# Kernel tuning notes

Hardware: AMD Instinct MI355X
Metric: run time of the kernel (lower is better)

The kernel has to match this reference:

```python
import jax, jax.numpy as jnp
import numpy as np
import math

D_MODEL = 1024
NUM_HEADS = 16
MAX_LEN = 2048
B, S = 2, 2048


def setup_inputs() -> dict:
    key = jax.random.key(0)
    ks = jax.random.split(key, 6)
    w_scale = 1.0 / math.sqrt(D_MODEL)  # ~xavier
    return {
        "x": jax.random.normal(ks[0], (B, S, D_MODEL), dtype=jnp.float32),
        "Wq": jax.random.normal(ks[1], (D_MODEL, D_MODEL), dtype=jnp.float32) * w_scale,
        "bq": jnp.zeros((D_MODEL,), dtype=jnp.float32),
        "Wk": jax.random.normal(ks[2], (D_MODEL, D_MODEL), dtype=jnp.float32) * w_scale,
        "bk": jnp.zeros((D_MODEL,), dtype=jnp.float32),
        "Wv": jax.random.normal(ks[3], (D_MODEL, D_MODEL), dtype=jnp.float32) * w_scale,
        "bv": jnp.zeros((D_MODEL,), dtype=jnp.float32),
        "Wo": jax.random.normal(ks[4], (D_MODEL, D_MODEL), dtype=jnp.float32) * w_scale,
        "bo": jnp.zeros((D_MODEL,), dtype=jnp.float32),
        "Er": jax.random.normal(ks[5], (MAX_LEN, D_MODEL // NUM_HEADS), dtype=jnp.float32),
    }


def reference(x, Wq, bq, Wk, bk, Wv, bv, Wo, bo, Er):
    Bsz, Sl, Dm = x.shape
    H = NUM_HEADS
    dqk = Dm // H

    def split_heads(z):
        # [B,S,D] -> [B,H,S,dqk]
        return z.reshape(Bsz, Sl, H, dqk).transpose(0, 2, 1, 3)

    Q = split_heads(x @ Wq.T + bq)
    K = split_heads(x @ Wk.T + bk)
    V = split_heads(x @ Wv.T + bv)

    Er_sl = Er[MAX_LEN - Sl:, :]  # [S, dqk]
    # Faithful to source: contract over d -> [B,H,S], unsqueeze last dim
    QEr = jnp.einsum('bhld,ld->bhl', Q, Er_sl)[..., None]  # [B,H,S,1]
    # skew(): pad left by 1 on last dim, reshape, drop first row
    padded = jnp.pad(QEr, ((0, 0), (0, 0), (0, 0), (1, 0)))  # [B,H,S,2]
    Srel = padded.reshape(Bsz, H, 2, Sl)[:, :, 1:, :]  # [B,H,1,S]

    QK_t = jnp.einsum('bhld,bhmd->bhlm', Q, K)  # [B,H,S,S]
    attn_scores = (QK_t + Srel) / math.sqrt(dqk)

    causal = jnp.tril(jnp.ones((Sl, Sl), dtype=bool))  # [S,S]
    attn_scores = jnp.where(causal[None, None], attn_scores, -jnp.inf)

    attn_probs = jax.nn.softmax(attn_scores, axis=-1)
    attn_out = jnp.einsum('bhlm,bhmd->bhld', attn_probs, V)  # [B,H,S,dqk]
    attn_out = attn_out.transpose(0, 2, 1, 3).reshape(Bsz, Sl, Dm)
    return attn_out @ Wo.T + bo  # dropout omitted (eval mode)
```

## Files before the change

kernel.cpp:

```cpp
#include <hip/hip_runtime.h>
#include <hip/hip_bf16.h>

#define D_MODEL 1024
#define NHEAD 16
#define DH 64
#define BSZ 2
#define SEQ 2048
#define MROWS (BSZ*SEQ)
#define SCL_Q 0.1803368801111204f
#define CHSZ 17408

typedef __attribute__((ext_vector_type(4))) float f32x4;
typedef __attribute__((ext_vector_type(8))) __bf16 bf16x8;
typedef __attribute__((ext_vector_type(8))) unsigned short u16x8;

__device__ __forceinline__ float b2f(unsigned short u) {
    union { unsigned int i; float f; } v; v.i = ((unsigned int)u) << 16; return v.f;
}
__device__ __forceinline__ unsigned short f2b(float f) {
    union { float f; unsigned int i; } v; v.f = f;
    unsigned int u = v.i;
    u += 0x7fffu + ((u >> 16) & 1u);
    return (unsigned short)(u >> 16);
}

#define GLDS16(gptr, lptr) \
    __builtin_amdgcn_global_load_lds((__attribute__((address_space(1))) void*)(gptr), \
                                     (__attribute__((address_space(3))) void*)(lptr), 16, 0, 0)

__global__ __launch_bounds__(256) void cvt5(
    const float* __restrict__ sx,
    const float* __restrict__ s1, const float* __restrict__ s2,
    const float* __restrict__ s3, const float* __restrict__ s4,
    unsigned short* __restrict__ dx,
    unsigned short* __restrict__ d1, unsigned short* __restrict__ d2,
    unsigned short* __restrict__ d3, unsigned short* __restrict__ d4)
{
    const int seg = blockIdx.y;
    const float* src; unsigned short* dst; int n4;
    if (seg == 0)      { src = sx; dst = dx; n4 = MROWS*D_MODEL/4; }
    else if (seg == 1) { src = s1; dst = d1; n4 = D_MODEL*D_MODEL/4; }
    else if (seg == 2) { src = s2; dst = d2; n4 = D_MODEL*D_MODEL/4; }
    else if (seg == 3) { src = s3; dst = d3; n4 = D_MODEL*D_MODEL/4; }
    else               { src = s4; dst = d4; n4 = D_MODEL*D_MODEL/4; }
    int i = blockIdx.x * 256 + threadIdx.x;
    int stride = gridDim.x * 256;
    for (; i < n4; i += stride) {
        float4 v = ((const float4*)src)[i];
        ushort4 o;
        o.x = f2b(v.x); o.y = f2b(v.y); o.z = f2b(v.z); o.w = f2b(v.w);
        ((ushort4*)dst)[i] = o;
    }
}

__global__ __launch_bounds__(256) void gemm_qkv(
    const unsigned short* __restrict__ X,
    const unsigned short* __restrict__ Wq, const unsigned short* __restrict__ Wk,
    const unsigned short* __restrict__ Wv,
    const float* __restrict__ bq, const float* __restrict__ bk, const float* __restrict__ bv,
    unsigned short* __restrict__ Qo, unsigned short* __restrict__ Ko, unsigned short* __restrict__ Vo)
{
    __shared__ unsigned short lsA[2][128*32];
    __shared__ unsigned short lsB[2][128*32];
    const int tid = threadIdx.x;
    const int z = blockIdx.z;
    const unsigned short* W = (z==0) ? Wq : (z==1) ? Wk : Wv;
    const float* bias = (z==0) ? bq : (z==1) ? bk : bv;
    unsigned short* Out = (z==0) ? Qo : (z==1) ? Ko : Vo;
    const int tM = blockIdx.y * 128;
    const int tN = blockIdx.x * 128;
    const int w = tid >> 6, lane = tid & 63;
    const int wr = w >> 1, wc = w & 1;
    const int lr = lane & 15, lk = lane >> 4;
    const f32x4 fz = {0.f, 0.f, 0.f, 0.f};
    f32x4 acc[4][4];
    #pragma unroll
    for (int m = 0; m < 4; m++)
        #pragma unroll
        for (int n = 0; n < 4; n++) acc[m][n] = fz;

    const int e0 = tid, e1 = 256 + tid;
    const int r0 = e0 >> 2, c0 = ((e0 & 3) ^ (r0 & 3)) * 8;
    const int r1 = e1 >> 2, c1 = ((e1 & 3) ^ (r1 & 3)) * 8;

#define GEMM_STAGE(buf, k0_) do { \
        GLDS16(X + (size_t)(tM + r0) * D_MODEL + (k0_) + c0, &lsA[buf][e0 * 8]); \
        GLDS16(X + (size_t)(tM + r1) * D_MODEL + (k0_) + c1, &lsA[buf][e1 * 8]); \
        GLDS16(W + (size_t)(tN + r0) * D_MODEL + (k0_) + c0, &lsB[buf][e0 * 8]); \
        GLDS16(W + (size_t)(tN + r1) * D_MODEL + (k0_) + c1, &lsB[buf][e1 * 8]); \
    } while (0)

    GEMM_STAGE(0, 0);
    __syncthreads();
    int cur = 0;
    for (int k0 = 0; k0 < D_MODEL; k0 += 32) {
        if (k0 + 32 < D_MODEL) GEMM_STAGE(cur ^ 1, k0 + 32);
        bf16x8 af[4], bfr[4];
        #pragma unroll
        for (int m = 0; m < 4; m++) {
            int row = wr*64 + m*16 + lr;
            af[m] = *(const bf16x8*)&lsA[cur][row*32 + ((lk ^ (row & 3)) * 8)];
        }
        #pragma unroll
        for (int n = 0; n < 4; n++) {
            int row = wc*64 + n*16 + lr;
            bfr[n] = *(const bf16x8*)&lsB[cur][row*32 + ((lk ^ (row & 3)) * 8)];
        }
        #pragma unroll
        for (int m = 0; m < 4; m++)
            #pragma unroll
            for (int n = 0; n < 4; n++)
                acc[m][n] = __builtin_amdgcn_mfma_f32_16x16x32_bf16(af[m], bfr[n], acc[m][n], 0, 0, 0);
        __syncthreads();
        cur ^= 1;
    }
#undef GEMM_STAGE
    const float qscl = (z == 0) ? SCL_Q : 1.0f;
    #pragma unroll
    for (int m = 0; m < 4; m++) {
        int ibase = tM + wr*64 + m*16 + lk*4;
        #pragma unroll
        for (int n = 0; n < 4; n++) {
            int j = tN + wc*64 + n*16 + lr;
            float bj = bias[j];
            int h = j >> 6, d = j & 63;
            #pragma unroll
            for (int r = 0; r < 4; r++) {
                int row = ibase + r;
                int b = row >> 11, s = row & 2047;
                Out[((size_t)(b*NHEAD + h) * SEQ + s) * DH + d] = f2b((acc[m][n][r] + bj) * qscl);
            }
        }
    }
}

__global__ __launch_bounds__(512) void gemm_out(
    const unsigned short* __restrict__ X, const unsigned short* __restrict__ W,
    const float* __restrict__ bias, float* __restrict__ Out)
{
    __shared__ unsigned short lsA[2][128*32];
    __shared__ unsigned short lsB[2][64*32];
    const int tid = threadIdx.x;
    const int tM = blockIdx.y * 128;
    const int tN = blockIdx.x * 64;
    const int w = tid >> 6, lane = tid & 63;
    const int wr = w >> 1, wc = w & 1;
    const int lr = lane & 15, lk = lane >> 4;
    const f32x4 fz = {0.f, 0.f, 0.f, 0.f};
    f32x4 acc[2][2];
    #pragma unroll
    for (int m = 0; m < 2; m++)
        #pragma unroll
        for (int n = 0; n < 2; n++) acc[m][n] = fz;

    const int ra = tid >> 2, ca = ((tid & 3) ^ (ra & 3)) * 8;
    const int eb = tid & 255;
    const int rb = eb >> 2, cb = ((eb & 3) ^ (rb & 3)) * 8;

#define OUT_STAGE(buf, k0_) do { \
        GLDS16(X + (size_t)(tM + ra) * D_MODEL + (k0_) + ca, &lsA[buf][tid * 8]); \
        if (tid < 256) GLDS16(W + (size_t)(tN + rb) * D_MODEL + (k0_) + cb, &lsB[buf][eb * 8]); \
    } while (0)

    OUT_STAGE(0, 0);
    __syncthreads();
    int cur = 0;
    for (int k0 = 0; k0 < D_MODEL; k0 += 32) {
        if (k0 + 32 < D_MODEL) OUT_STAGE(cur ^ 1, k0 + 32);
        bf16x8 af[2], bfr[2];
        #pragma unroll
        for (int m = 0; m < 2; m++) {
            int row = wr*32 + m*16 + lr;
            af[m] = *(const bf16x8*)&lsA[cur][row*32 + ((lk ^ (row & 3)) * 8)];
        }
        #pragma unroll
        for (int n = 0; n < 2; n++) {
            int row = wc*32 + n*16 + lr;
            bfr[n] = *(const bf16x8*)&lsB[cur][row*32 + ((lk ^ (row & 3)) * 8)];
        }
        #pragma unroll
        for (int m = 0; m < 2; m++)
            #pragma unroll
            for (int n = 0; n < 2; n++)
                acc[m][n] = __builtin_amdgcn_mfma_f32_16x16x32_bf16(af[m], bfr[n], acc[m][n], 0, 0, 0);
        __syncthreads();
        cur ^= 1;
    }
#undef OUT_STAGE
    #pragma unroll
    for (int m = 0; m < 2; m++) {
        int ibase = tM + wr*32 + m*16 + lk*4;
        #pragma unroll
        for (int n = 0; n < 2; n++) {
            int j = tN + wc*32 + n*16 + lr;
            float bj = bias[j];
            #pragma unroll
            for (int r = 0; r < 4; r++)
                Out[(size_t)(ibase + r) * D_MODEL + j] = acc[m][n][r] + bj;
        }
    }
}

__global__ __launch_bounds__(256) void vtrans(const unsigned short* __restrict__ V,
                                              unsigned short* __restrict__ Vt) {
    __shared__ unsigned short t[64][80];
    const int bh = blockIdx.y;
    const int s0 = blockIdx.x * 64;
    const int tid = threadIdx.x;
    #pragma unroll
    for (int i = 0; i < 2; i++) {
        int e = i*256 + tid;
        int r = e >> 3, c = e & 7;
        u16x8 v = *(const u16x8*)&V[((size_t)bh * SEQ + s0 + r) * DH + c*8];
        *(u16x8*)&t[r][c*8] = v;
    }
    __syncthreads();
    #pragma unroll
    for (int i = 0; i < 2; i++) {
        int e = i*256 + tid;
        int d = e >> 3, c = e & 7;
        u16x8 o;
        #pragma unroll
        for (int j = 0; j < 8; j++) o[j] = t[c*8 + j][d];
        *(u16x8*)&Vt[((size_t)bh * DH + d) * SEQ + s0 + c*8] = o;
    }
}

__global__ __launch_bounds__(256) void qer_k(const unsigned short* __restrict__ Q,
                                             const float* __restrict__ Er,
                                             float* __restrict__ qer) {
    int gw = blockIdx.x * 4 + (threadIdx.x >> 6);
    int lane = threadIdx.x & 63;
    int l = gw & (SEQ - 1);
    float p = b2f(Q[(size_t)gw * DH + lane]) * Er[l * DH + lane];
    #pragma unroll
    for (int m = 32; m >= 1; m >>= 1) p += __shfl_xor(p, m, 64);
    if (lane == 0) qer[gw] = p;
}

__global__ __launch_bounds__(512) void attn_k(
    const unsigned short* __restrict__ Q, const unsigned short* __restrict__ Kg,
    const unsigned short* __restrict__ Vt, const float* __restrict__ qer,
    unsigned short* __restrict__ Om, char* __restrict__ part)
{
    __shared__ unsigned short lsK[2][64*64];
    __shared__ unsigned short lsV[2][64*64];
    __shared__ unsigned short lsP[128*64];
    const unsigned char tab[24] = {
        (7<<2),        (15<<2)|2, (15<<2)|3, (14<<2)|2, (14<<2)|3,
        (6<<2),        (13<<2)|2, (13<<2)|3, (12<<2)|2, (12<<2)|3,
        (5<<2),        (11<<2)|2, (11<<2)|3, (10<<2)|2, (10<<2)|3,
        (4<<2),        (9<<2)|2,  (9<<2)|3,  (8<<2)|2,  (8<<2)|3,
        (3<<2), (2<<2), (1<<2), (0<<2)
    };
    const int id = blockIdx.x;
    const int bh = id & 31;
    const int v = tab[id >> 5];
    const int j = v >> 2;
    const bool split = (v >> 1) & 1;
    const int half = v & 1;
    const int kt0 = (split && half) ? (j + 1) : 0;
    const int ktN = (split && !half) ? (j + 1) : (2*j + 2);
    const int b = bh >> 4, h = bh & 15;
    const int tid = threadIdx.x;
    const int w = tid >> 6, lane = tid & 63;
    const int lr = lane & 15, lk = lane >> 4;
    const int q = w*16 + lr;
    const int qrow = j*128 + q;
    const f32x4 fz = {0.f, 0.f, 0.f, 0.f};

    const unsigned short* Qrow = Q + ((size_t)bh * SEQ + qrow) * DH;
    bf16x8 bq0 = *(const bf16x8*)&Qrow[lk*8];
    bf16x8 bq1 = *(const bf16x8*)&Qrow[32 + lk*8];

    const int sr = tid >> 3, sc = ((tid & 7) ^ (sr & 7)) * 8;
    const unsigned short* kst = Kg + ((size_t)bh * SEQ + kt0*64 + sr) * DH + sc;
    const unsigned short* vst = Vt + ((size_t)bh * DH + sr) * SEQ + kt0*64 + sc;
    const float* qb = qer + (size_t)bh * SEQ + 1024 + kt0*32 + lk*2;

#define ATTN_STAGE(buf) do { \
        GLDS16(kst, &lsK[buf][tid * 8]); kst += 64*DH; \
        GLDS16(vst, &lsV[buf][tid * 8]); vst += 64; \
    } while (0)

    f32x4 o[4];
    #pragma unroll
    for (int df = 0; df < 4; df++) o[df] = fz;
    float mrun = -3.0e38f, lsum = 0.0f;

    ATTN_STAGE(0);
    __syncthreads();
    int cur = 0;

    for (int kt = kt0; kt < ktN; kt++) {
        if (kt + 1 < ktN) ATTN_STAGE(cur ^ 1);
        float2 bv[4];
        #pragma unroll
        for (int kf = 0; kf < 4; kf++) bv[kf] = *(const float2*)(qb + kf*8);
        qb += 32;
        float st[4][4];
        __builtin_amdgcn_s_setprio(1);
        #pragma unroll
        for (int kf = 0; kf < 4; kf++) {
            int row = kf*16 + lr;
            bf16x8 a0 = *(const bf16x8*)&lsK[cur][row*64 + ((lk ^ (row & 7)) * 8)];
            bf16x8 a1 = *(const bf16x8*)&lsK[cur][row*64 + (((4 + lk) ^ (row & 7)) * 8)];
            f32x4 zv = fz;
            zv = __builtin_amdgcn_mfma_f32_16x16x32_bf16(a0, bq0, zv, 0, 0, 0);
            zv = __builtin_amdgcn_mfma_f32_16x16x32_bf16(a1, bq1, zv, 0, 0, 0);
            st[kf][0] = zv[0];
            st[kf][1] = zv[1] + bv[kf].x;
            st[kf][2] = zv[2];
            st[kf][3] = zv[3] + bv[kf].y;
        }
        __builtin_amdgcn_s_setprio(0);
        if (kt >= 2*j) {
            #pragma unroll
            for (int kf = 0; kf < 4; kf++) {
                int kg0 = kt*64 + kf*16 + lk*4;
                #pragma unroll
                for (int r = 0; r < 4; r++)
                    if (kg0 + r > qrow) st[kf][r] = -3.0e38f;
            }
        }
        float pm = st[0][0];
        #pragma unroll
        for (int kf = 0; kf < 4; kf++)
            #pragma unroll
            for (int r = 0; r < 4; r++) pm = fmaxf(pm, st[kf][r]);
        pm = fmaxf(pm, __shfl_xor(pm, 16, 64));
        pm = fmaxf(pm, __shfl_xor(pm, 32, 64));
        if (pm > mrun + 8.0f) {
            float sc8 = exp2f(mrun - pm);
            mrun = pm;
            lsum *= sc8;
            #pragma unroll
            for (int df = 0; df < 4; df++)
                #pragma unroll
                for (int r = 0; r < 4; r++) o[df][r] *= sc8;
        }
        float p[4][4];
        float rs = 0.0f;
        #pragma unroll
        for (int kf = 0; kf < 4; kf++)
            #pragma unroll
            for (int r = 0; r < 4; r++) {
                p[kf][r] = exp2f(st[kf][r] - mrun);
                rs += p[kf][r];
            }
        rs += __shfl_xor(rs, 16, 64);
        rs += __shfl_xor(rs, 32, 64);
        lsum += rs;
        #pragma unroll
        for (int kf = 0; kf < 4; kf++) {
            union { __hip_bfloat162 h2[2]; unsigned long long u; } pk;
            pk.h2[0] = __float22bfloat162_rn(float2{p[kf][0], p[kf][1]});
            pk.h2[1] = __float22bfloat162_rn(float2{p[kf][2], p[kf][3]});
            *(unsigned long long*)&lsP[q*64 + ((((kf<<2)|lk) ^ ((lr&7)<<1))<<2)] = pk.u;
        }
        bf16x8 pb0 = *(const bf16x8*)&lsP[q*64 + ((lk ^ (lr&7))<<3)];
        bf16x8 pb1 = *(const bf16x8*)&lsP[q*64 + (((4+lk) ^ (lr&7))<<3)];
        __builtin_amdgcn_s_setprio(1);
        #pragma unroll
        for (int df = 0; df < 4; df++) {
            int row = df*16 + lr;
            bf16x8 v0 = *(const bf16x8*)&lsV[cur][row*64 + ((lk ^ (row & 7)) * 8)];
            bf16x8 v1 = *(const bf16x8*)&lsV[cur][row*64 + (((4 + lk) ^ (row & 7)) * 8)];
            o[df] = __builtin_amdgcn_mfma_f32_16x16x32_bf16(v0, pb0, o[df], 0, 0, 0);
            o[df] = __builtin_amdgcn_mfma_f32_16x16x32_bf16(v1, pb1, o[df], 0, 0, 0);
        }
        __builtin_amdgcn_s_setprio(0);
        __syncthreads();
        cur ^= 1;
    }
#undef ATTN_STAGE
    if (split) {
        char* cb = part + (size_t)((bh*8 + (j - 8))*2 + half) * CHSZ;
        unsigned short* ob = (unsigned short*)cb;
        #pragma unroll
        for (int df = 0; df < 4; df++) {
            ushort4 ov;
            ov.x = f2b(o[df][0]); ov.y = f2b(o[df][1]);
            ov.z = f2b(o[df][2]); ov.w = f2b(o[df][3]);
            *(ushort4*)&ob[q*64 + df*16 + lk*4] = ov;
        }
        float* ml = (float*)(cb + 16384);
        if (lk == 0) { ml[q] = mrun; ml[128 + q] = lsum; }
    } else {
        float inv = 1.0f / lsum;
        #pragma unroll
        for (int df = 0; df < 4; df++) {
            ushort4 ov;
            ov.x = f2b(o[df][0] * inv);
            ov.y = f2b(o[df][1] * inv);
            ov.z = f2b(o[df][2] * inv);
            ov.w = f2b(o[df][3] * inv);
            *(ushort4*)&Om[((size_t)(b * SEQ + qrow)) * D_MODEL + h*64 + df*16 + lk*4] = ov;
        }
    }
}

__global__ __launch_bounds__(256) void attn_merge(const char* __restrict__ part,
                                                  unsigned short* __restrict__ Om)
{
    const int bh = blockIdx.x & 31, jj = blockIdx.x >> 5;
    const int b = bh >> 4, h = bh & 15, j = 8 + jj;
    const char* c0 = part + (size_t)((bh*8 + jj)*2) * CHSZ;
    const char* c1 = c0 + CHSZ;
    const unsigned short* o0 = (const unsigned short*)c0;
    const unsigned short* o1 = (const unsigned short*)c1;
    const float* ml0 = (const float*)(c0 + 16384);
    const float* ml1 = (const float*)(c1 + 16384);
    const int t = threadIdx.x;
    const int q = t >> 1, dh = (t & 1) * 32;
    float m0 = ml0[q], l0 = ml0[128 + q];
    float m1 = ml1[q], l1 = ml1[128 + q];
    float M = fmaxf(m0, m1);
    float w0 = exp2f(m0 - M), w1 = exp2f(m1 - M);
    float inv = 1.0f / (l0 * w0 + l1 * w1);
    w0 *= inv; w1 *= inv;
    unsigned short* dst = Om + ((size_t)(b*SEQ + j*128 + q)) * D_MODEL + h*64 + dh;
    #pragma unroll
    for (int i = 0; i < 4; i++) {
        u16x8 a = *(const u16x8*)&o0[q*64 + dh + i*8];
        u16x8 c = *(const u16x8*)&o1[q*64 + dh + i*8];
        u16x8 ov;
        #pragma unroll
        for (int r = 0; r < 8; r++)
            ov[r] = f2b(b2f(a[r])*w0 + b2f(c[r])*w1);
        *(u16x8*)&dst[i*8] = ov;
    }
}

extern "C" void kernel_launch(void* const* d_in, const int* in_sizes, int n_in,
                              void* d_out, int out_size, void* d_ws, size_t ws_size,
                              hipStream_t stream) {
    const float* x  = (const float*)d_in[0];
    const float* Wq = (const float*)d_in[1];
    const float* bq = (const float*)d_in[2];
    const float* Wk = (const float*)d_in[3];
    const float* bk = (const float*)d_in[4];
    const float* Wv = (const float*)d_in[5];
    const float* bv = (const float*)d_in[6];
    const float* Wo = (const float*)d_in[7];
    const float* bo = (const float*)d_in[8];
    const float* Er = (const float*)d_in[9];

    char* ws = (char*)d_ws;
    const size_t MB = 1024*1024;
    unsigned short* xb  = (unsigned short*)(ws);
    unsigned short* Wqb = (unsigned short*)(ws + 8*MB);
    unsigned short* Wkb = (unsigned short*)(ws + 10*MB);
    unsigned short* Wvb = (unsigned short*)(ws + 12*MB);
    unsigned short* Wob = (unsigned short*)(ws + 14*MB);
    unsigned short* Qb  = (unsigned short*)(ws + 16*MB);
    unsigned short* Kb  = (unsigned short*)(ws + 24*MB);
    unsigned short* Vb  = (unsigned short*)(ws + 32*MB);
    unsigned short* Vtb = (unsigned short*)(ws + 40*MB);
    float* qer          = (float*)(ws + 48*MB);
    char*  part         = (char*)(ws + 48*MB + 262144);

    cvt5<<<dim3(1024, 5), 256, 0, stream>>>(x, Wq, Wk, Wv, Wo, xb, Wqb, Wkb, Wvb, Wob);

    gemm_qkv<<<dim3(8, 32, 3), 256, 0, stream>>>(xb, Wqb, Wkb, Wvb, bq, bk, bv, Qb, Kb, Vb);
    vtrans<<<dim3(32, 32), 256, 0, stream>>>(Vb, Vtb);
    qer_k<<<16384, 256, 0, stream>>>(Qb, Er, qer);
    attn_k<<<768, 512, 0, stream>>>(Qb, Kb, Vtb, qer, xb, part);
    attn_merge<<<256, 256, 0, stream>>>(part, xb);
    gemm_out<<<dim3(16, 32), 512, 0, stream>>>(xb, Wob, bo, (float*)d_out);
}
```

Measured before the change: 133.6 us.

## Process two 16-row query groups per wave in attention with 256-thread blocks

```diff
diff --git a/kernel.cpp b/kernel.cpp
--- a/kernel.cpp
+++ b/kernel.cpp
@@ -238,7 +238,7 @@
     if (lane == 0) qer[gw] = p;
 }
 
-__global__ __launch_bounds__(512) void attn_k(
+__global__ __launch_bounds__(256, 3) void attn_k(
     const unsigned short* __restrict__ Q, const unsigned short* __restrict__ Kg,
     const unsigned short* __restrict__ Vt, const float* __restrict__ qer,
     unsigned short* __restrict__ Om, char* __restrict__ part)
@@ -265,28 +265,36 @@
     const int tid = threadIdx.x;
     const int w = tid >> 6, lane = tid & 63;
     const int lr = lane & 15, lk = lane >> 4;
-    const int q = w*16 + lr;
-    const int qrow = j*128 + q;
+    const int q0 = w*32 + lr, q1 = q0 + 16;
+    const int qrow0 = j*128 + q0, qrow1 = qrow0 + 16;
     const f32x4 fz = {0.f, 0.f, 0.f, 0.f};
 
-    const unsigned short* Qrow = Q + ((size_t)bh * SEQ + qrow) * DH;
-    bf16x8 bq0 = *(const bf16x8*)&Qrow[lk*8];
-    bf16x8 bq1 = *(const bf16x8*)&Qrow[32 + lk*8];
-
-    const int sr = tid >> 3, sc = ((tid & 7) ^ (sr & 7)) * 8;
-    const unsigned short* kst = Kg + ((size_t)bh * SEQ + kt0*64 + sr) * DH + sc;
-    const unsigned short* vst = Vt + ((size_t)bh * DH + sr) * SEQ + kt0*64 + sc;
+    const unsigned short* Qr0 = Q + ((size_t)bh * SEQ + qrow0) * DH;
+    const unsigned short* Qr1 = Q + ((size_t)bh * SEQ + qrow1) * DH;
+    bf16x8 bqa0 = *(const bf16x8*)&Qr0[lk*8];
+    bf16x8 bqa1 = *(const bf16x8*)&Qr0[32 + lk*8];
+    bf16x8 bqb0 = *(const bf16x8*)&Qr1[lk*8];
+    bf16x8 bqb1 = *(const bf16x8*)&Qr1[32 + lk*8];
+
+    const int sr0 = tid >> 3,          sc0 = ((tid & 7) ^ (sr0 & 7)) * 8;
+    const int sr1 = (256 + tid) >> 3,  sc1 = (((256 + tid) & 7) ^ (sr1 & 7)) * 8;
+    const unsigned short* kst0 = Kg + ((size_t)bh * SEQ + kt0*64 + sr0) * DH + sc0;
+    const unsigned short* kst1 = Kg + ((size_t)bh * SEQ + kt0*64 + sr1) * DH + sc1;
+    const unsigned short* vst0 = Vt + ((size_t)bh * DH + sr0) * SEQ + kt0*64 + sc0;
+    const unsigned short* vst1 = Vt + ((size_t)bh * DH + sr1) * SEQ + kt0*64 + sc1;
     const float* qb = qer + (size_t)bh * SEQ + 1024 + kt0*32 + lk*2;
 
 #define ATTN_STAGE(buf) do { \
-        GLDS16(kst, &lsK[buf][tid * 8]); kst += 64*DH; \
-        GLDS16(vst, &lsV[buf][tid * 8]); vst += 64; \
+        GLDS16(kst0, &lsK[buf][tid * 8]);        kst0 += 64*DH; \
+        GLDS16(kst1, &lsK[buf][(256+tid) * 8]);  kst1 += 64*DH; \
+        GLDS16(vst0, &lsV[buf][tid * 8]);        vst0 += 64; \
+        GLDS16(vst1, &lsV[buf][(256+tid) * 8]);  vst1 += 64; \
     } while (0)
 
-    f32x4 o[4];
-    #pragma unroll
-    for (int df = 0; df < 4; df++) o[df] = fz;
-    float mrun = -3.0e38f, lsum = 0.0f;
+    f32x4 o0[4], o1[4];
+    #pragma unroll
+    for (int df = 0; df < 4; df++) { o0[df] = fz; o1[df] = fz; }
+    float m0 = -3.0e38f, l0 = 0.0f, m1 = -3.0e38f, l1 = 0.0f;
 
     ATTN_STAGE(0);
     __syncthreads();
@@ -298,20 +306,26 @@
         #pragma unroll
         for (int kf = 0; kf < 4; kf++) bv[kf] = *(const float2*)(qb + kf*8);
         qb += 32;
-        float st[4][4];
+        float st[4][4], su[4][4];
         __builtin_amdgcn_s_setprio(1);
         #pragma unroll
         for (int kf = 0; kf < 4; kf++) {
             int row = kf*16 + lr;
             bf16x8 a0 = *(const bf16x8*)&lsK[cur][row*64 + ((lk ^ (row & 7)) * 8)];
             bf16x8 a1 = *(const bf16x8*)&lsK[cur][row*64 + (((4 + lk) ^ (row & 7)) * 8)];
-            f32x4 zv = fz;
-            zv = __builtin_amdgcn_mfma_f32_16x16x32_bf16(a0, bq0, zv, 0, 0, 0);
-            zv = __builtin_amdgcn_mfma_f32_16x16x32_bf16(a1, bq1, zv, 0, 0, 0);
+            f32x4 zv = fz, yv = fz;
+            zv = __builtin_amdgcn_mfma_f32_16x16x32_bf16(a0, bqa0, zv, 0, 0, 0);
+            zv = __builtin_amdgcn_mfma_f32_16x16x32_bf16(a1, bqa1, zv, 0, 0, 0);
+            yv = __builtin_amdgcn_mfma_f32_16x16x32_bf16(a0, bqb0, yv, 0, 0, 0);
+            yv = __builtin_amdgcn_mfma_f32_16x16x32_bf16(a1, bqb1, yv, 0, 0, 0);
             st[kf][0] = zv[0];
             st[kf][1] = zv[1] + bv[kf].x;
             st[kf][2] = zv[2];
             st[kf][3] = zv[3] + bv[kf].y;
+            su[kf][0] = yv[0];
+            su[kf][1] = yv[1] + bv[kf].x;
+            su[kf][2] = yv[2];
+            su[kf][3] = yv[3] + bv[kf].y;
         }
         __builtin_amdgcn_s_setprio(0);
         if (kt >= 2*j) {
@@ -319,55 +333,92 @@
             for (int kf = 0; kf < 4; kf++) {
                 int kg0 = kt*64 + kf*16 + lk*4;
                 #pragma unroll
-                for (int r = 0; r < 4; r++)
-                    if (kg0 + r > qrow) st[kf][r] = -3.0e38f;
+                for (int r = 0; r < 4; r++) {
+                    if (kg0 + r > qrow0) st[kf][r] = -3.0e38f;
+                    if (kg0 + r > qrow1) su[kf][r] = -3.0e38f;
+                }
             }
         }
-        float pm = st[0][0];
-        #pragma unroll
-        for (int kf = 0; kf < 4; kf++)
-            #pragma unroll
-            for (int r = 0; r < 4; r++) pm = fmaxf(pm, st[kf][r]);
-        pm = fmaxf(pm, __shfl_xor(pm, 16, 64));
-        pm = fmaxf(pm, __shfl_xor(pm, 32, 64));
-        if (pm > mrun + 8.0f) {
-            float sc8 = exp2f(mrun - pm);
-            mrun = pm;
-            lsum *= sc8;
-            #pragma unroll
-            for (int df = 0; df < 4; df++)
+        {
+            float pm = st[0][0];
+            #pragma unroll
+            for (int kf = 0; kf < 4; kf++)
                 #pragma unroll
-                for (int r = 0; r < 4; r++) o[df][r] *= sc8;
-        }
-        float p[4][4];
-        float rs = 0.0f;
-        #pragma unroll
-        for (int kf = 0; kf < 4; kf++)
-            #pragma unroll
-            for (int r = 0; r < 4; r++) {
-                p[kf][r] = exp2f(st[kf][r] - mrun);
-                rs += p[kf][r];
+                for (int r = 0; r < 4; r++) pm = fmaxf(pm, st[kf][r]);
+            pm = fmaxf(pm, __shfl_xor(pm, 16, 64));
+            pm = fmaxf(pm, __shfl_xor(pm, 32, 64));
+            if (pm > m0 + 8.0f) {
+                float sc8 = exp2f(m0 - pm);
+                m0 = pm; l0 *= sc8;
+                #pragma unroll
+                for (int df = 0; df < 4; df++)
+                    #pragma unroll
+                    for (int r = 0; r < 4; r++) o0[df][r] *= sc8;
             }
-        rs += __shfl_xor(rs, 16, 64);
-        rs += __shfl_xor(rs, 32, 64);
-        lsum += rs;
-        #pragma unroll
-        for (int kf = 0; kf < 4; kf++) {
-            union { __hip_bfloat162 h2[2]; unsigned long long u; } pk;
-            pk.h2[0] = __float22bfloat162_rn(float2{p[kf][0], p[kf][1]});
-            pk.h2[1] = __float22bfloat162_rn(float2{p[kf][2], p[kf][3]});
-            *(unsigned long long*)&lsP[q*64 + ((((kf<<2)|lk) ^ ((lr&7)<<1))<<2)] = pk.u;
-        }
-        bf16x8 pb0 = *(const bf16x8*)&lsP[q*64 + ((lk ^ (lr&7))<<3)];
-        bf16x8 pb1 = *(const bf16x8*)&lsP[q*64 + (((4+lk) ^ (lr&7))<<3)];
+            float rs = 0.0f;
+            #pragma unroll
+            for (int kf = 0; kf < 4; kf++) {
+                float p0 = exp2f(st[kf][0] - m0);
+                float p1 = exp2f(st[kf][1] - m0);
+                float p2 = exp2f(st[kf][2] - m0);
+                float p3 = exp2f(st[kf][3] - m0);
+                rs += (p0 + p1) + (p2 + p3);
+                union { __hip_bfloat162 h2[2]; unsigned long long u; } pk;
+                pk.h2[0] = __float22bfloat162_rn(float2{p0, p1});
+                pk.h2[1] = __float22bfloat162_rn(float2{p2, p3});
+                *(unsigned long long*)&lsP[q0*64 + ((((kf<<2)|lk) ^ ((lr&7)<<1))<<2)] = pk.u;
+            }
+            rs += __shfl_xor(rs, 16, 64);
+            rs += __shfl_xor(rs, 32, 64);
+            l0 += rs;
+        }
+        {
+            float pm = su[0][0];
+            #pragma unroll
+            for (int kf = 0; kf < 4; kf++)
+                #pragma unroll
+                for (int r = 0; r < 4; r++) pm = fmaxf(pm, su[kf][r]);
+            pm = fmaxf(pm, __shfl_xor(pm, 16, 64));
+            pm = fmaxf(pm, __shfl_xor(pm, 32, 64));
+            if (pm > m1 + 8.0f) {
+                float sc8 = exp2f(m1 - pm);
+                m1 = pm; l1 *= sc8;
+                #pragma unroll
+                for (int df = 0; df < 4; df++)
+                    #pragma unroll
+                    for (int r = 0; r < 4; r++) o1[df][r] *= sc8;
+            }
+            float rs = 0.0f;
+            #pragma unroll
+            for (int kf = 0; kf < 4; kf++) {
+                float p0 = exp2f(su[kf][0] - m1);
+                float p1 = exp2f(su[kf][1] - m1);
+                float p2 = exp2f(su[kf][2] - m1);
+                float p3 = exp2f(su[kf][3] - m1);
+                rs += (p0 + p1) + (p2 + p3);
+                union { __hip_bfloat162 h2[2]; unsigned long long u; } pk;
+                pk.h2[0] = __float22bfloat162_rn(float2{p0, p1});
+                pk.h2[1] = __float22bfloat162_rn(float2{p2, p3});
+                *(unsigned long long*)&lsP[q1*64 + ((((kf<<2)|lk) ^ ((lr&7)<<1))<<2)] = pk.u;
+            }
+            rs += __shfl_xor(rs, 16, 64);
+            rs += __shfl_xor(rs, 32, 64);
+            l1 += rs;
+        }
+        bf16x8 pa0 = *(const bf16x8*)&lsP[q0*64 + ((lk ^ (lr&7))<<3)];
+        bf16x8 pa1 = *(const bf16x8*)&lsP[q0*64 + (((4+lk) ^ (lr&7))<<3)];
+        bf16x8 pb0 = *(const bf16x8*)&lsP[q1*64 + ((lk ^ (lr&7))<<3)];
+        bf16x8 pb1 = *(const bf16x8*)&lsP[q1*64 + (((4+lk) ^ (lr&7))<<3)];
         __builtin_amdgcn_s_setprio(1);
         #pragma unroll
         for (int df = 0; df < 4; df++) {
             int row = df*16 + lr;
             bf16x8 v0 = *(const bf16x8*)&lsV[cur][row*64 + ((lk ^ (row & 7)) * 8)];
             bf16x8 v1 = *(const bf16x8*)&lsV[cur][row*64 + (((4 + lk) ^ (row & 7)) * 8)];
-            o[df] = __builtin_amdgcn_mfma_f32_16x16x32_bf16(v0, pb0, o[df], 0, 0, 0);
-            o[df] = __builtin_amdgcn_mfma_f32_16x16x32_bf16(v1, pb1, o[df], 0, 0, 0);
+            o0[df] = __builtin_amdgcn_mfma_f32_16x16x32_bf16(v0, pa0, o0[df], 0, 0, 0);
+            o0[df] = __builtin_amdgcn_mfma_f32_16x16x32_bf16(v1, pa1, o0[df], 0, 0, 0);
+            o1[df] = __builtin_amdgcn_mfma_f32_16x16x32_bf16(v0, pb0, o1[df], 0, 0, 0);
+            o1[df] = __builtin_amdgcn_mfma_f32_16x16x32_bf16(v1, pb1, o1[df], 0, 0, 0);
         }
         __builtin_amdgcn_s_setprio(0);
         __syncthreads();
@@ -380,22 +431,33 @@
         #pragma unroll
         for (int df = 0; df < 4; df++) {
             ushort4 ov;
-            ov.x = f2b(o[df][0]); ov.y = f2b(o[df][1]);
-            ov.z = f2b(o[df][2]); ov.w = f2b(o[df][3]);
-            *(ushort4*)&ob[q*64 + df*16 + lk*4] = ov;
+            ov.x = f2b(o0[df][0]); ov.y = f2b(o0[df][1]);
+            ov.z = f2b(o0[df][2]); ov.w = f2b(o0[df][3]);
+            *(ushort4*)&ob[q0*64 + df*16 + lk*4] = ov;
+            ov.x = f2b(o1[df][0]); ov.y = f2b(o1[df][1]);
+            ov.z = f2b(o1[df][2]); ov.w = f2b(o1[df][3]);
+            *(ushort4*)&ob[q1*64 + df*16 + lk*4] = ov;
         }
         float* ml = (float*)(cb + 16384);
-        if (lk == 0) { ml[q] = mrun; ml[128 + q] = lsum; }
+        if (lk == 0) {
+            ml[q0] = m0; ml[128 + q0] = l0;
+            ml[q1] = m1; ml[128 + q1] = l1;
+        }
     } else {
-        float inv = 1.0f / lsum;
+        float inv0 = 1.0f / l0, inv1 = 1.0f / l1;
         #pragma unroll
         for (int df = 0; df < 4; df++) {
             ushort4 ov;
-            ov.x = f2b(o[df][0] * inv);
-            ov.y = f2b(o[df][1] * inv);
-            ov.z = f2b(o[df][2] * inv);
-            ov.w = f2b(o[df][3] * inv);
-            *(ushort4*)&Om[((size_t)(b * SEQ + qrow)) * D_MODEL + h*64 + df*16 + lk*4] = ov;
+            ov.x = f2b(o0[df][0] * inv0);
+            ov.y = f2b(o0[df][1] * inv0);
+            ov.z = f2b(o0[df][2] * inv0);
+            ov.w = f2b(o0[df][3] * inv0);
+            *(ushort4*)&Om[((size_t)(b * SEQ + qrow0)) * D_MODEL + h*64 + df*16 + lk*4] = ov;
+            ov.x = f2b(o1[df][0] * inv1);
+            ov.y = f2b(o1[df][1] * inv1);
+            ov.z = f2b(o1[df][2] * inv1);
+            ov.w = f2b(o1[df][3] * inv1);
+            *(ushort4*)&Om[((size_t)(b * SEQ + qrow1)) * D_MODEL + h*64 + df*16 + lk*4] = ov;
         }
     }
 }
@@ -465,7 +527,7 @@
     gemm_qkv<<<dim3(8, 32, 3), 256, 0, stream>>>(xb, Wqb, Wkb, Wvb, bq, bk, bv, Qb, Kb, Vb);
     vtrans<<<dim3(32, 32), 256, 0, stream>>>(Vb, Vtb);
     qer_k<<<16384, 256, 0, stream>>>(Qb, Er, qer);
-    attn_k<<<768, 512, 0, stream>>>(Qb, Kb, Vtb, qer, xb, part);
+    attn_k<<<768, 256, 0, stream>>>(Qb, Kb, Vtb, qer, xb, part);
     attn_merge<<<256, 256, 0, stream>>>(part, xb);
     gemm_out<<<dim3(16, 32), 512, 0, stream>>>(xb, Wob, bo, (float*)d_out);
 }
```

After: 127.4 us. 1.05x faster.
